# Kernel tuning notes

Hardware: AMD Instinct MI355X
Metric: run time of the kernel (lower is better)

Reference implementation:

```python
import jax, jax.numpy as jnp
import numpy as np

NEG = -1.0e9  # matches the -1000000000.0 masking constant in the torch source


def setup_inputs() -> dict:
    key = jax.random.key(0)
    k1, k2, k3, k4 = jax.random.split(key, 4)
    B, N, M, D = 32, 2048, 512, 128
    sequence1 = jax.random.normal(k1, (B, N, D), dtype=jnp.float32)
    sequence2 = jax.random.normal(k2, (B, M, D), dtype=jnp.float32)
    sequence1_mask = jax.random.randint(k3, (B, N), 0, 2, dtype=jnp.int32)
    sequence2_mask = jax.random.randint(k4, (B, M), 0, 2, dtype=jnp.int32)
    return {
        "sequence1": sequence1,
        "sequence2": sequence2,
        "sequence1_mask": sequence1_mask,
        "sequence2_mask": sequence2_mask,
    }


def reference(sequence1, sequence2, sequence1_mask, sequence2_mask):
    # sequence1: [B, n, d] (context), sequence2: [B, m, d] (question)
    dt = sequence1.dtype
    m1 = sequence1_mask.astype(dt)  # [B, n]
    m2 = sequence2_mask.astype(dt)  # [B, m]

    # DotProduct similarity over the (virtually) tiled tensors -> [B, n, m].
    # Fused: no [B,n,m,d] intermediates.
    S = jnp.einsum('bnd,bmd->bnm', sequence1, sequence2)

    # masked softmax over sequence2 positions (context-to-question attention)
    a2 = jax.nn.softmax(S + (1.0 - m2)[:, None, :] * NEG, axis=-1)  # [B, n, m]
    seq1_seq2_attention = jnp.einsum('bnm,bmd->bnd', a2, sequence2)

    # one-shot question-to-context attention: masked max over m, softmax over n
    s1 = jnp.max(S * m2[:, None, :] + (1.0 - m2)[:, None, :] * NEG, axis=-1)  # [B, n]
    a1 = jax.nn.softmax(s1 + (1.0 - m1) * NEG, axis=-1)  # [B, n]
    seq2_seq1_attention = jnp.einsum('bn,bnd->bd', a1, sequence1)  # [B, d]

    return (seq1_seq2_attention, a2, seq2_seq1_attention, a1)
```

## Files before the change

kernel.cpp:

```cpp
#include <hip/hip_runtime.h>
#include <stdint.h>

#define NEGC (-1.0e9f)

typedef __attribute__((ext_vector_type(8))) short bf16x8;
typedef __attribute__((ext_vector_type(4))) float f32x4;

__device__ __align__(16) unsigned short g_S2H[32u * 512u * 128u];
__device__ __align__(16) unsigned short g_S2L[32u * 512u * 128u];
__device__ __align__(16) unsigned short g_VT[32u * 128u * 512u];

__device__ __forceinline__ unsigned short f2bf(float f) {
    union { float f; unsigned int u; } v; v.f = f;
    unsigned int r = v.u + 0x7fffu + ((v.u >> 16) & 1u);
    return (unsigned short)(r >> 16);
}
__device__ __forceinline__ float bf2f(unsigned short h) {
    union { float f; unsigned int u; } v; v.u = ((unsigned int)h) << 16;
    return v.f;
}

__device__ __forceinline__ void gl_lds16(const void* g, void* l) {
    __builtin_amdgcn_global_load_lds(
        (const __attribute__((address_space(1))) unsigned int*)g,
        (__attribute__((address_space(3))) unsigned int*)l, 16, 0, 0);
}

__global__ __launch_bounds__(256) void k_prep(const float* __restrict__ seq2) {
    __shared__ unsigned short Lh[32 * 130];
    const int b = blockIdx.x >> 4, c = blockIdx.x & 15, t = threadIdx.x;
    const int m0 = c * 32;

    const float4* src = (const float4*)(seq2 + (size_t)(b * 512 + m0) * 128);
    ushort4* dh = (ushort4*)(g_S2H + (size_t)(b * 512 + m0) * 128);
    ushort4* dl = (ushort4*)(g_S2L + (size_t)(b * 512 + m0) * 128);
#pragma unroll
    for (int p = 0; p < 4; ++p) {
        int idx = p * 256 + t;
        int row = idx >> 5, c4 = idx & 31;
        float4 v = src[idx];
        float vs[4] = {v.x, v.y, v.z, v.w};
        unsigned short hh[4], ll[4];
#pragma unroll
        for (int i = 0; i < 4; ++i) { hh[i] = f2bf(vs[i]); ll[i] = f2bf(vs[i] - bf2f(hh[i])); }
        ushort4 uh{hh[0], hh[1], hh[2], hh[3]};
        ushort4 ul{ll[0], ll[1], ll[2], ll[3]};
        dh[idx] = uh;
        dl[idx] = ul;
#pragma unroll
        for (int i = 0; i < 4; ++i) Lh[row * 130 + c4 * 4 + i] = hh[i];
    }
    __syncthreads();

    const int d = t >> 1, sub = t & 1;
    unsigned short pk[16];
#pragma unroll
    for (int j = 0; j < 16; ++j) pk[j] = Lh[(sub * 16 + j) * 130 + d];
    unsigned short* dst = g_VT + (size_t)(b * 128 + d) * 512 + m0 + sub * 16;
    *(bf16x8*)dst = *(bf16x8*)pk;
    *(bf16x8*)(dst + 8) = *(bf16x8*)(pk + 8);
}

#define KBASE 16384
#define TBASE 32768
#define M2OFF 49152
#define REDOFF 49664
#define LDS_TOTAL 50176

__global__ __launch_bounds__(256, 3) void bidir_main(
    const float* __restrict__ seq1,
    const int* __restrict__ m1, const int* __restrict__ m2,
    float* __restrict__ out0, float* __restrict__ a2out,
    float* __restrict__ a1log)
{
    __shared__ __align__(16) char smem[LDS_TOTAL];

    const int t = threadIdx.x, lane = t & 63, w = t >> 6;
    const int wr = w >> 1, wc = w & 1, q = lane >> 4, fr = lane & 15;
    const int orig = blockIdx.x;
    const int swzb = (orig & 7) * 256 + (orig >> 3);
    const int b = swzb >> 6, n0 = (swzb & 63) << 5;

    unsigned char* M2u8 = (unsigned char*)(smem + M2OFF);
    float* REDm = (float*)(smem + REDOFF);
    float* REDs = (float*)(smem + REDOFF + 256);

    {
        const unsigned short* sb = (w < 2) ? g_S2H : g_S2L;
        const char* srcb = (const char*)(sb + (size_t)(b * 512 + (w & 1) * 256) * 128);
        char* dstb = smem + KBASE + w * 8192;
#pragma unroll
        for (int i = 0; i < 8; ++i) {
            int r = i * 4 + q;
            int so = r * 256 + ((fr * 16) ^ ((r & 7) << 4));
            gl_lds16(srcb + so, dstb + i * 1024);
        }
    }

    if (t < 128) {
        int4 v = ((const int4*)(m2 + b * 512))[t];
        uchar4 u{(unsigned char)v.x, (unsigned char)v.y, (unsigned char)v.z, (unsigned char)v.w};
        *(uchar4*)(M2u8 + t * 4) = u;
    }
    {
        const float4* s1p = (const float4*)(seq1 + (size_t)(b * 2048 + n0) * 128);
#pragma unroll
        for (int p = 0; p < 4; ++p) {
            int idx = p * 256 + t;
            int row = idx >> 5, c4 = idx & 31;
            float4 v = s1p[idx];
            float vs[4] = {v.x, v.y, v.z, v.w};
            unsigned short hh[4], ll[4];
#pragma unroll
            for (int i = 0; i < 4; ++i) { hh[i] = f2bf(vs[i]); ll[i] = f2bf(vs[i] - bf2f(hh[i])); }
            ushort4 uh{hh[0], hh[1], hh[2], hh[3]};
            ushort4 ul{ll[0], ll[1], ll[2], ll[3]};
            int off = (row * 256 + c4 * 8) ^ ((row & 7) << 4);
            *(ushort4*)(smem + off) = uh;
            *(ushort4*)(smem + 8192 + off) = ul;
        }
    }
    __syncthreads();

    bf16x8 ah[4], al[4];
    {
        int row = wr * 16 + fr;
        int sw = (row & 7) << 4;
#pragma unroll
        for (int ks = 0; ks < 4; ++ks) {
            int off = (row * 256 + ks * 64 + q * 16) ^ sw;
            ah[ks] = *(const bf16x8*)(smem + off);
            al[ks] = *(const bf16x8*)(smem + 8192 + off);
        }
    }

    f32x4 acc[8][2];
#pragma unroll
    for (int i = 0; i < 8; ++i) {
        acc[i][0] = (f32x4){0.f, 0.f, 0.f, 0.f};
        acc[i][1] = (f32x4){0.f, 0.f, 0.f, 0.f};
    }

#pragma unroll
    for (int mt = 0; mt < 8; ++mt) {
        if (mt > 0) {
            const unsigned short* sb = (w < 2) ? g_S2H : g_S2L;
            const char* srcb = (const char*)(sb + (size_t)(b * 512 + (w & 1) * 256 + mt * 32) * 128);
            char* dstb = smem + KBASE + w * 8192;
#pragma unroll
            for (int i = 0; i < 8; ++i) {
                int r = i * 4 + q;
                int so = r * 256 + ((fr * 16) ^ ((r & 7) << 4));
                gl_lds16(srcb + so, dstb + i * 1024);
            }
        }
        __syncthreads();
        {
            const char* KH = smem + KBASE + wc * 8192;
            const char* KL = smem + KBASE + 16384 + wc * 8192;
#pragma unroll
            for (int s = 0; s < 2; ++s) {
                int rrow = s * 16 + fr;
                int sw = (fr & 7) << 4;
#pragma unroll
                for (int ks = 0; ks < 4; ++ks) {
                    int off = (rrow * 256 + ks * 64 + q * 16) ^ sw;
                    bf16x8 bh = *(const bf16x8*)(KH + off);
                    bf16x8 bl = *(const bf16x8*)(KL + off);
                    acc[mt][s] = __builtin_amdgcn_mfma_f32_16x16x32_bf16(al[ks], bh, acc[mt][s], 0, 0, 0);
                    acc[mt][s] = __builtin_amdgcn_mfma_f32_16x16x32_bf16(ah[ks], bl, acc[mt][s], 0, 0, 0);
                    acc[mt][s] = __builtin_amdgcn_mfma_f32_16x16x32_bf16(ah[ks], bh, acc[mt][s], 0, 0, 0);
                }
            }
        }
        __syncthreads();
    }

#pragma unroll
    for (int mt = 0; mt < 8; ++mt)
#pragma unroll
        for (int s = 0; s < 2; ++s) {
            int m = wc * 256 + mt * 32 + s * 16 + fr;
            bool keep = M2u8[m] != 0;
#pragma unroll
            for (int r = 0; r < 4; ++r)
                acc[mt][s][r] = keep ? acc[mt][s][r] : NEGC;
        }
    float rmax[4];
#pragma unroll
    for (int r = 0; r < 4; ++r) rmax[r] = NEGC;
#pragma unroll
    for (int mt = 0; mt < 8; ++mt)
#pragma unroll
        for (int s = 0; s < 2; ++s)
#pragma unroll
            for (int r = 0; r < 4; ++r) rmax[r] = fmaxf(rmax[r], acc[mt][s][r]);
#pragma unroll
    for (int off = 1; off < 16; off <<= 1)
#pragma unroll
        for (int r = 0; r < 4; ++r) rmax[r] = fmaxf(rmax[r], __shfl_xor(rmax[r], off));
    if (fr == 0) {
#pragma unroll
        for (int r = 0; r < 4; ++r) REDm[wc * 32 + wr * 16 + q * 4 + r] = rmax[r];
    }
    __syncthreads();
    float RM[4];
#pragma unroll
    for (int r = 0; r < 4; ++r) {
        int rl = wr * 16 + q * 4 + r;
        RM[r] = fmaxf(REDm[rl], REDm[32 + rl]);
    }
    if (t < 32) {
        float v = fmaxf(REDm[t], REDm[32 + t]);
        float m1v = (float)m1[b * 2048 + n0 + t];
        a1log[b * 2048 + n0 + t] = v + (1.0f - m1v) * NEGC;
    }
    float rs[4] = {0.f, 0.f, 0.f, 0.f};
#pragma unroll
    for (int mt = 0; mt < 8; ++mt)
#pragma unroll
        for (int s = 0; s < 2; ++s)
#pragma unroll
            for (int r = 0; r < 4; ++r) {
                float e = __expf(acc[mt][s][r] - RM[r]);
                acc[mt][s][r] = e;
                rs[r] += e;
            }
#pragma unroll
    for (int off = 1; off < 16; off <<= 1)
#pragma unroll
        for (int r = 0; r < 4; ++r) rs[r] += __shfl_xor(rs[r], off);
    if (fr == 0) {
#pragma unroll
        for (int r = 0; r < 4; ++r) REDs[wc * 32 + wr * 16 + q * 4 + r] = rs[r];
    }
    __syncthreads();
    float rinv[4];
#pragma unroll
    for (int r = 0; r < 4; ++r) {
        int rl = wr * 16 + q * 4 + r;
        rinv[r] = 1.0f / (REDs[rl] + REDs[32 + rl]);
    }

    {
        char* dstb = smem + TBASE + w * 4096;
#pragma unroll
        for (int i = 0; i < 4; ++i) {
            int d = w * 32 + i * 8 + (lane >> 3);
            int cb = (lane & 7) * 16;
            size_t so = (size_t)(b * 128 + d) * 1024 + (cb ^ ((d & 7) << 4));
            gl_lds16((const char*)g_VT + so, dstb + i * 1024);
        }
    }

#pragma unroll
    for (int mt = 0; mt < 8; ++mt)
#pragma unroll
        for (int s = 0; s < 2; ++s) {
            int m = wc * 256 + mt * 32 + s * 16 + fr;
#pragma unroll
            for (int r = 0; r < 4; ++r) {
                int rl = wr * 16 + q * 4 + r;
                float v = acc[mt][s][r] * rinv[r];
                __builtin_nontemporal_store(v, &a2out[(size_t)(b * 2048 + n0 + rl) * 512 + m]);
                int off = (rl * 1024 + m * 2) ^ ((rl & 7) << 4);
                *(unsigned short*)(smem + off) = f2bf(v);
            }
        }

    f32x4 oacc[4];
#pragma unroll
    for (int c = 0; c < 4; ++c) oacc[c] = (f32x4){0.f, 0.f, 0.f, 0.f};

#pragma unroll
    for (int mt = 0; mt < 8; ++mt) {
        if (mt > 0) {
            char* dstb = smem + TBASE + w * 4096;
#pragma unroll
            for (int i = 0; i < 4; ++i) {
                int d = w * 32 + i * 8 + (lane >> 3);
                int cb = (lane & 7) * 16;
                size_t so = (size_t)(b * 128 + d) * 1024 + mt * 128 + (cb ^ ((d & 7) << 4));
                gl_lds16((const char*)g_VT + so, dstb + i * 1024);
            }
        }
        __syncthreads();
        {
            int arow = wr * 16 + fr;
            int asw = (fr & 7) << 4;
#pragma unroll
            for (int ks = 0; ks < 2; ++ks) {
                int aoff = (arow * 1024 + mt * 128 + ks * 64 + q * 16) ^ asw;
                bf16x8 pa = *(const bf16x8*)(smem + aoff);
#pragma unroll
                for (int c = 0; c < 4; ++c) {
                    int d = wc * 64 + c * 16 + fr;
                    int boff = (d * 128 + ks * 64 + q * 16) ^ ((d & 7) << 4);
                    bf16x8 bv = *(const bf16x8*)(smem + TBASE + boff);
                    oacc[c] = __builtin_amdgcn_mfma_f32_16x16x32_bf16(pa, bv, oacc[c], 0, 0, 0);
                }
            }
        }
        __syncthreads();
    }

#pragma unroll
    for (int c = 0; c < 4; ++c)
#pragma unroll
        for (int r = 0; r < 4; ++r) {
            int rl = wr * 16 + q * 4 + r;
            int d = wc * 64 + c * 16 + fr;
            __builtin_nontemporal_store(oacc[c][r], &out0[(size_t)(b * 2048 + n0 + rl) * 128 + d]);
        }
}

__global__ __launch_bounds__(256) void k_a1(float* __restrict__ a1slot,
                                            float* __restrict__ out2) {
    __shared__ float wred[4];
    const int b = blockIdx.x, t = threadIdx.x, lane = t & 63, w = t >> 6;

    if (t < 128) out2[b * 128 + t] = 0.f;

    const float4* Lp = (const float4*)(a1slot + (size_t)b * 2048);
    float4 La = Lp[t * 2], Lb = Lp[t * 2 + 1];
    float l[8] = {La.x, La.y, La.z, La.w, Lb.x, Lb.y, Lb.z, Lb.w};

    float lmax = l[0];
#pragma unroll
    for (int j = 1; j < 8; ++j) lmax = fmaxf(lmax, l[j]);
#pragma unroll
    for (int off = 1; off < 64; off <<= 1) lmax = fmaxf(lmax, __shfl_xor(lmax, off));
    if (lane == 0) wred[w] = lmax;
    __syncthreads();
    float bmax = fmaxf(fmaxf(wred[0], wred[1]), fmaxf(wred[2], wred[3]));

    float e[8]; float s = 0.f;
#pragma unroll
    for (int j = 0; j < 8; ++j) { e[j] = __expf(l[j] - bmax); s += e[j]; }
#pragma unroll
    for (int off = 1; off < 64; off <<= 1) s += __shfl_xor(s, off);
    __syncthreads();
    if (lane == 0) wred[w] = s;
    __syncthreads();
    float inv = 1.0f / (wred[0] + wred[1] + wred[2] + wred[3]);

    float4 o1{e[0] * inv, e[1] * inv, e[2] * inv, e[3] * inv};
    float4 o2v{e[4] * inv, e[5] * inv, e[6] * inv, e[7] * inv};
    ((float4*)(a1slot + (size_t)b * 2048))[t * 2] = o1;
    ((float4*)(a1slot + (size_t)b * 2048))[t * 2 + 1] = o2v;
}

__global__ __launch_bounds__(256) void k_gemv(const float* __restrict__ seq1,
                                              const float* __restrict__ a1,
                                              float* __restrict__ out2) {
    __shared__ float a1b[256];
    __shared__ float4 red[8][32];
    const int bid = blockIdx.x, b = bid >> 3, ch = bid & 7, t = threadIdx.x;
    const int n0 = ch * 256;
    if (t < 64) ((float4*)a1b)[t] = ((const float4*)(a1 + (size_t)b * 2048 + n0))[t];
    __syncthreads();
    const int d4 = t & 31, sl = t >> 5;
    float4 acc{0.f, 0.f, 0.f, 0.f};
    const float4* s1 = (const float4*)(seq1 + (size_t)(b * 2048 + n0 + sl * 32) * 128);
#pragma unroll 8
    for (int j = 0; j < 32; ++j) {
        float wv = a1b[sl * 32 + j];
        float4 v = s1[j * 32 + d4];
        acc.x += wv * v.x; acc.y += wv * v.y; acc.z += wv * v.z; acc.w += wv * v.w;
    }
    red[sl][d4] = acc;
    __syncthreads();
    if (t < 32) {
        float4 s0 = red[0][t];
#pragma unroll
        for (int c = 1; c < 8; ++c) {
            float4 v = red[c][t];
            s0.x += v.x; s0.y += v.y; s0.z += v.z; s0.w += v.w;
        }
        float* dst = out2 + b * 128 + t * 4;
        atomicAdd(dst + 0, s0.x);
        atomicAdd(dst + 1, s0.y);
        atomicAdd(dst + 2, s0.z);
        atomicAdd(dst + 3, s0.w);
    }
}

extern "C" void kernel_launch(void* const* d_in, const int* in_sizes, int n_in,
                              void* d_out, int out_size, void* d_ws, size_t ws_size,
                              hipStream_t stream) {
    const float* seq1 = (const float*)d_in[0];
    const float* seq2 = (const float*)d_in[1];
    const int*   m1   = (const int*)d_in[2];
    const int*   m2   = (const int*)d_in[3];
    (void)d_ws; (void)ws_size; (void)n_in; (void)in_sizes;

    float* out  = (float*)d_out;
    float* out0 = out;
    float* a2o  = out + 8388608;
    float* o2   = out + 41943040;
    float* a1o  = out + 41947136;

    k_prep<<<dim3(512), dim3(256), 0, stream>>>(seq2);
    bidir_main<<<dim3(2048), dim3(256), 0, stream>>>(seq1, m1, m2, out0, a2o, a1o);
    k_a1<<<dim3(32), dim3(256), 0, stream>>>(a1o, o2);
    k_gemv<<<dim3(256), dim3(256), 0, stream>>>(seq1, a1o, o2);
}
```

Before: 95.84 us.

## Load MFMA operands directly from global memory instead of staging through LDS

Removes the LDS staging of the K (split bf16 seq2) and V^T tiles. MFMA B operands are now read straight from global/L2 in per-lane bf16x8 loads, and seq1 is converted to hi/lo bf16 in registers without passing through LDS. This drops most __syncthreads barriers and shrinks LDS use, which could raise occupancy. The cost is that the four waves no longer share operand loads, so global/L2 traffic per block goes up, and nontemporal stores are swapped for plain stores.

```diff
diff --git a/kernel.cpp b/kernel.cpp
--- a/kernel.cpp
+++ b/kernel.cpp
@@ -18,12 +18,6 @@
 __device__ __forceinline__ float bf2f(unsigned short h) {
     union { float f; unsigned int u; } v; v.u = ((unsigned int)h) << 16;
     return v.f;
-}
-
-__device__ __forceinline__ void gl_lds16(const void* g, void* l) {
-    __builtin_amdgcn_global_load_lds(
-        (const __attribute__((address_space(1))) unsigned int*)g,
-        (__attribute__((address_space(3))) unsigned int*)l, 16, 0, 0);
 }
 
 __global__ __launch_bounds__(256) void k_prep(const float* __restrict__ seq2) {
@@ -61,11 +55,9 @@
     *(bf16x8*)(dst + 8) = *(bf16x8*)(pk + 8);
 }
 
-#define KBASE 16384
-#define TBASE 32768
-#define M2OFF 49152
-#define REDOFF 49664
-#define LDS_TOTAL 50176
+#define M2OFF 32768
+#define REDOFF 33280
+#define LDS_TOTAL 33792
 
 __global__ __launch_bounds__(256, 3) void bidir_main(
     const float* __restrict__ seq1,
@@ -85,52 +77,25 @@
     float* REDm = (float*)(smem + REDOFF);
     float* REDs = (float*)(smem + REDOFF + 256);
 
-    {
-        const unsigned short* sb = (w < 2) ? g_S2H : g_S2L;
-        const char* srcb = (const char*)(sb + (size_t)(b * 512 + (w & 1) * 256) * 128);
-        char* dstb = smem + KBASE + w * 8192;
-#pragma unroll
-        for (int i = 0; i < 8; ++i) {
-            int r = i * 4 + q;
-            int so = r * 256 + ((fr * 16) ^ ((r & 7) << 4));
-            gl_lds16(srcb + so, dstb + i * 1024);
-        }
-    }
-
     if (t < 128) {
         int4 v = ((const int4*)(m2 + b * 512))[t];
         uchar4 u{(unsigned char)v.x, (unsigned char)v.y, (unsigned char)v.z, (unsigned char)v.w};
         *(uchar4*)(M2u8 + t * 4) = u;
     }
-    {
-        const float4* s1p = (const float4*)(seq1 + (size_t)(b * 2048 + n0) * 128);
-#pragma unroll
-        for (int p = 0; p < 4; ++p) {
-            int idx = p * 256 + t;
-            int row = idx >> 5, c4 = idx & 31;
-            float4 v = s1p[idx];
-            float vs[4] = {v.x, v.y, v.z, v.w};
-            unsigned short hh[4], ll[4];
-#pragma unroll
-            for (int i = 0; i < 4; ++i) { hh[i] = f2bf(vs[i]); ll[i] = f2bf(vs[i] - bf2f(hh[i])); }
-            ushort4 uh{hh[0], hh[1], hh[2], hh[3]};
-            ushort4 ul{ll[0], ll[1], ll[2], ll[3]};
-            int off = (row * 256 + c4 * 8) ^ ((row & 7) << 4);
-            *(ushort4*)(smem + off) = uh;
-            *(ushort4*)(smem + 8192 + off) = ul;
-        }
-    }
-    __syncthreads();
 
     bf16x8 ah[4], al[4];
     {
-        int row = wr * 16 + fr;
-        int sw = (row & 7) << 4;
+        const float* qp = seq1 + (size_t)(b * 2048 + n0 + wr * 16 + fr) * 128;
 #pragma unroll
         for (int ks = 0; ks < 4; ++ks) {
-            int off = (row * 256 + ks * 64 + q * 16) ^ sw;
-            ah[ks] = *(const bf16x8*)(smem + off);
-            al[ks] = *(const bf16x8*)(smem + 8192 + off);
+            float4 v0 = *(const float4*)(qp + ks * 32 + q * 8);
+            float4 v1 = *(const float4*)(qp + ks * 32 + q * 8 + 4);
+            float vs[8] = {v0.x, v0.y, v0.z, v0.w, v1.x, v1.y, v1.z, v1.w};
+            unsigned short hh[8], ll[8];
+#pragma unroll
+            for (int j = 0; j < 8; ++j) { hh[j] = f2bf(vs[j]); ll[j] = f2bf(vs[j] - bf2f(hh[j])); }
+            ah[ks] = *(bf16x8*)hh;
+            al[ks] = *(bf16x8*)ll;
         }
     }
 
@@ -141,40 +106,26 @@
         acc[i][1] = (f32x4){0.f, 0.f, 0.f, 0.f};
     }
 
-#pragma unroll
-    for (int mt = 0; mt < 8; ++mt) {
-        if (mt > 0) {
-            const unsigned short* sb = (w < 2) ? g_S2H : g_S2L;
-            const char* srcb = (const char*)(sb + (size_t)(b * 512 + (w & 1) * 256 + mt * 32) * 128);
-            char* dstb = smem + KBASE + w * 8192;
-#pragma unroll
-            for (int i = 0; i < 8; ++i) {
-                int r = i * 4 + q;
-                int so = r * 256 + ((fr * 16) ^ ((r & 7) << 4));
-                gl_lds16(srcb + so, dstb + i * 1024);
-            }
-        }
-        __syncthreads();
-        {
-            const char* KH = smem + KBASE + wc * 8192;
-            const char* KL = smem + KBASE + 16384 + wc * 8192;
+    {
+        const unsigned short* baseH = g_S2H + (size_t)(b * 512 + wc * 256) * 128 + q * 8;
+        const unsigned short* baseL = g_S2L + (size_t)(b * 512 + wc * 256) * 128 + q * 8;
+#pragma unroll
+        for (int mt = 0; mt < 8; ++mt)
 #pragma unroll
             for (int s = 0; s < 2; ++s) {
-                int rrow = s * 16 + fr;
-                int sw = (fr & 7) << 4;
+                const unsigned short* rH = baseH + (size_t)(mt * 32 + s * 16 + fr) * 128;
+                const unsigned short* rL = baseL + (size_t)(mt * 32 + s * 16 + fr) * 128;
 #pragma unroll
                 for (int ks = 0; ks < 4; ++ks) {
-                    int off = (rrow * 256 + ks * 64 + q * 16) ^ sw;
-                    bf16x8 bh = *(const bf16x8*)(KH + off);
-                    bf16x8 bl = *(const bf16x8*)(KL + off);
+                    bf16x8 bh = *(const bf16x8*)(rH + ks * 32);
+                    bf16x8 bl = *(const bf16x8*)(rL + ks * 32);
                     acc[mt][s] = __builtin_amdgcn_mfma_f32_16x16x32_bf16(al[ks], bh, acc[mt][s], 0, 0, 0);
                     acc[mt][s] = __builtin_amdgcn_mfma_f32_16x16x32_bf16(ah[ks], bl, acc[mt][s], 0, 0, 0);
                     acc[mt][s] = __builtin_amdgcn_mfma_f32_16x16x32_bf16(ah[ks], bh, acc[mt][s], 0, 0, 0);
                 }
             }
-        }
-        __syncthreads();
-    }
+    }
+    __syncthreads();
 
 #pragma unroll
     for (int mt = 0; mt < 8; ++mt)
@@ -242,17 +193,6 @@
         rinv[r] = 1.0f / (REDs[rl] + REDs[32 + rl]);
     }
 
-    {
-        char* dstb = smem + TBASE + w * 4096;
-#pragma unroll
-        for (int i = 0; i < 4; ++i) {
-            int d = w * 32 + i * 8 + (lane >> 3);
-            int cb = (lane & 7) * 16;
-            size_t so = (size_t)(b * 128 + d) * 1024 + (cb ^ ((d & 7) << 4));
-            gl_lds16((const char*)g_VT + so, dstb + i * 1024);
-        }
-    }
-
 #pragma unroll
     for (int mt = 0; mt < 8; ++mt)
 #pragma unroll
@@ -262,46 +202,32 @@
             for (int r = 0; r < 4; ++r) {
                 int rl = wr * 16 + q * 4 + r;
                 float v = acc[mt][s][r] * rinv[r];
-                __builtin_nontemporal_store(v, &a2out[(size_t)(b * 2048 + n0 + rl) * 512 + m]);
+                a2out[(size_t)(b * 2048 + n0 + rl) * 512 + m] = v;
                 int off = (rl * 1024 + m * 2) ^ ((rl & 7) << 4);
                 *(unsigned short*)(smem + off) = f2bf(v);
             }
         }
+    __syncthreads();
 
     f32x4 oacc[4];
 #pragma unroll
     for (int c = 0; c < 4; ++c) oacc[c] = (f32x4){0.f, 0.f, 0.f, 0.f};
 
-#pragma unroll
-    for (int mt = 0; mt < 8; ++mt) {
-        if (mt > 0) {
-            char* dstb = smem + TBASE + w * 4096;
-#pragma unroll
-            for (int i = 0; i < 4; ++i) {
-                int d = w * 32 + i * 8 + (lane >> 3);
-                int cb = (lane & 7) * 16;
-                size_t so = (size_t)(b * 128 + d) * 1024 + mt * 128 + (cb ^ ((d & 7) << 4));
-                gl_lds16((const char*)g_VT + so, dstb + i * 1024);
+    {
+        const int arow = wr * 16 + fr;
+        const int asw = (fr & 7) << 4;
+        const unsigned short* vbase = g_VT + (size_t)(b * 128) * 512 + q * 8;
+#pragma unroll
+        for (int kt = 0; kt < 16; ++kt) {
+            int aoff = (arow * 1024 + kt * 64 + q * 16) ^ asw;
+            bf16x8 pa = *(const bf16x8*)(smem + aoff);
+#pragma unroll
+            for (int c = 0; c < 4; ++c) {
+                int d = wc * 64 + c * 16 + fr;
+                bf16x8 bv = *(const bf16x8*)(vbase + (size_t)d * 512 + kt * 32);
+                oacc[c] = __builtin_amdgcn_mfma_f32_16x16x32_bf16(pa, bv, oacc[c], 0, 0, 0);
             }
         }
-        __syncthreads();
-        {
-            int arow = wr * 16 + fr;
-            int asw = (fr & 7) << 4;
-#pragma unroll
-            for (int ks = 0; ks < 2; ++ks) {
-                int aoff = (arow * 1024 + mt * 128 + ks * 64 + q * 16) ^ asw;
-                bf16x8 pa = *(const bf16x8*)(smem + aoff);
-#pragma unroll
-                for (int c = 0; c < 4; ++c) {
-                    int d = wc * 64 + c * 16 + fr;
-                    int boff = (d * 128 + ks * 64 + q * 16) ^ ((d & 7) << 4);
-                    bf16x8 bv = *(const bf16x8*)(smem + TBASE + boff);
-                    oacc[c] = __builtin_amdgcn_mfma_f32_16x16x32_bf16(pa, bv, oacc[c], 0, 0, 0);
-                }
-            }
-        }
-        __syncthreads();
     }
 
 #pragma unroll
@@ -310,7 +236,7 @@
         for (int r = 0; r < 4; ++r) {
             int rl = wr * 16 + q * 4 + r;
             int d = wc * 64 + c * 16 + fr;
-            __builtin_nontemporal_store(oacc[c][r], &out0[(size_t)(b * 2048 + n0 + rl) * 128 + d]);
+            out0[(size_t)(b * 2048 + n0 + rl) * 128 + d] = oacc[c][r];
         }
 }
 
```

Result: slower. 206.6 us (+115.6%).
